# Performance work log

Hardware: AMD Instinct MI355X
Metric: run time of the kernel (lower is better)

Reference implementation:

```python
import jax, jax.numpy as jnp
import numpy as np

N_NODES = 100000
N_EDGES = 1600000
H_DIM = 64  # pos(32) + vel(32)


def _mlp_init(key, d_in, d_hid, d_out):
    k1, k2 = jax.random.split(key)
    s1 = 1.0 / np.sqrt(d_in)
    s2 = 1.0 / np.sqrt(d_hid)
    w1 = jax.random.uniform(k1, (d_in, d_hid), jnp.float32, -s1, s1)
    w2 = jax.random.uniform(k2, (d_hid, d_out), jnp.float32, -s2, s2)
    return w1, jnp.zeros((d_hid,), jnp.float32), w2, jnp.zeros((d_out,), jnp.float32)


def setup_inputs() -> dict:
    key = jax.random.key(0)
    ks = jax.random.split(key, 6)
    pos = jax.random.normal(ks[0], (N_NODES, 32), jnp.float32)
    vel = jax.random.normal(ks[1], (N_NODES, 32), jnp.float32)
    edge_index = jax.random.randint(ks[2], (2, N_EDGES), 0, N_NODES, jnp.int32)
    msg_w1, msg_b1, msg_w2, msg_b2 = _mlp_init(ks[3], 2 * H_DIM, 64, 64)
    upd_w1, upd_b1, upd_w2, upd_b2 = _mlp_init(ks[4], H_DIM + 64, 64, 64)
    sp = 1.0 / np.sqrt(64)
    pred_w = jax.random.uniform(ks[5], (64, 32), jnp.float32, -sp, sp)
    pred_b = jnp.zeros((32,), jnp.float32)
    return dict(pos=pos, vel=vel, edge_index=edge_index,
                msg_w1=msg_w1, msg_b1=msg_b1, msg_w2=msg_w2, msg_b2=msg_b2,
                upd_w1=upd_w1, upd_b1=upd_b1, upd_w2=upd_w2, upd_b2=upd_b2,
                pred_w=pred_w, pred_b=pred_b)


def reference(pos, vel, edge_index,
              msg_w1, msg_b1, msg_w2, msg_b2,
              upd_w1, upd_b1, upd_w2, upd_b2,
              pred_w, pred_b):
    n = pos.shape[0]
    h = jnp.concatenate([pos, vel], axis=-1)              # [N, 64]
    src, dst = edge_index[0], edge_index[1]
    h_i = h[dst]                                          # [E, 64] target nodes
    h_j = h[src]                                          # [E, 64] source nodes
    # message MLP on concat(h_i, h_j)
    m = jnp.concatenate([h_i, h_j], axis=-1)              # [E, 128]
    m = jax.nn.relu(m @ msg_w1 + msg_b1) @ msg_w2 + msg_b2  # [E, 64]
    # scatter-add aggregate to target nodes
    aggr = jax.ops.segment_sum(m, dst, num_segments=n)    # [N, 64]
    # update MLP on concat(h, aggr)
    u = jnp.concatenate([h, aggr], axis=-1)               # [N, 128]
    u = jax.nn.relu(u @ upd_w1 + upd_b1) @ upd_w2 + upd_b2  # [N, 64]
    # linear prediction head -> acceleration
    return u @ pred_w + pred_b                            # [N, 32]
```

## Files before the change

kernel.cpp:

```cpp
#include <hip/hip_runtime.h>

#define NN 100000
#define NE 1600000
#define SB   391
#define NBKT 391
#define EPB  4096

typedef _Float16 f16x8 __attribute__((ext_vector_type(8)));
typedef float    f32x4 __attribute__((ext_vector_type(4)));

#define ZB   1563
#define PHB  3125
#define PWB  13

extern "C" __global__ void __launch_bounds__(256)
prep_kernel(const float* __restrict__ pos, const float* __restrict__ vel,
            const int* __restrict__ ei,
            const float* __restrict__ mw1, const float* __restrict__ mw2,
            const float* __restrict__ uw1, const float* __restrict__ uw2,
            const float* __restrict__ pw,
            _Float16* __restrict__ hh,
            _Float16* __restrict__ mw1f, _Float16* __restrict__ mw2f,
            _Float16* __restrict__ uw1f, _Float16* __restrict__ uw2f,
            _Float16* __restrict__ pwf,
            float* __restrict__ aggr, int* __restrict__ cntm)
{
    __shared__ int lh[NBKT];
    const int b = blockIdx.x, tid = threadIdx.x;
    if (b < ZB) {
        float4* p = (float4*)aggr;
        const int base4 = b * 1024 + tid;
        const float4 z = make_float4(0.f, 0.f, 0.f, 0.f);
#pragma unroll
        for (int k = 0; k < 4; ++k) {
            const int idx = base4 + k * 256;
            if (idx < NN * 16) p[idx] = z;
        }
    } else if (b < ZB + PHB) {
        const int t = (b - ZB) * 256 + tid;
        const int node = t >> 3, seg = t & 7;
        const float* src = (seg < 4) ? pos + (size_t)node * 32 + seg * 8
                                     : vel + (size_t)node * 32 + (seg - 4) * 8;
        const float4 a = ((const float4*)src)[0];
        const float4 c = ((const float4*)src)[1];
        f16x8 r;
        r[0]=(_Float16)a.x; r[1]=(_Float16)a.y; r[2]=(_Float16)a.z; r[3]=(_Float16)a.w;
        r[4]=(_Float16)c.x; r[5]=(_Float16)c.y; r[6]=(_Float16)c.z; r[7]=(_Float16)c.w;
        *(f16x8*)(hh + (size_t)node * 64 + seg * 8) = r;
    } else if (b < ZB + PHB + PWB) {
        const int t2 = (b - ZB - PHB) * 256 + tid;
        if (t2 < 1024) {
            const int t = t2 >> 8, kk = (t2 >> 6) & 3, l = t2 & 63;
            f16x8 r;
#pragma unroll
            for (int j = 0; j < 8; ++j)
                r[j] = (_Float16)mw1[(kk * 32 + (l >> 4) * 8 + j) * 64 + t * 16 + (l & 15)];
            *(f16x8*)(mw1f + (size_t)t2 * 8) = r;
        } else if (t2 < 1536) {
            const int i = t2 - 1024;
            const int t = i >> 7, kk = (i >> 6) & 1, l = i & 63;
            f16x8 r;
#pragma unroll
            for (int j = 0; j < 8; ++j)
                r[j] = (_Float16)mw2[(kk * 32 + (l >> 4) * 8 + j) * 64 + t * 16 + (l & 15)];
            *(f16x8*)(mw2f + (size_t)i * 8) = r;
        } else if (t2 < 2560) {
            const int i = t2 - 1536;
            const int t = i >> 8, kk = (i >> 6) & 3, l = i & 63;
            f16x8 r;
#pragma unroll
            for (int j = 0; j < 8; ++j)
                r[j] = (_Float16)uw1[(kk * 32 + (l >> 4) * 8 + j) * 64 + t * 16 + (l & 15)];
            *(f16x8*)(uw1f + (size_t)i * 8) = r;
        } else if (t2 < 3072) {
            const int i = t2 - 2560;
            const int t = i >> 7, kk = (i >> 6) & 1, l = i & 63;
            f16x8 r;
#pragma unroll
            for (int j = 0; j < 8; ++j)
                r[j] = (_Float16)uw2[(kk * 32 + (l >> 4) * 8 + j) * 64 + t * 16 + (l & 15)];
            *(f16x8*)(uw2f + (size_t)i * 8) = r;
        } else if (t2 < 3328) {
            const int i = t2 - 3072;
            const int t = i >> 7, kk = (i >> 6) & 1, l = i & 63;
            f16x8 r;
#pragma unroll
            for (int j = 0; j < 8; ++j)
                r[j] = (_Float16)pw[(kk * 32 + (l >> 4) * 8 + j) * 32 + t * 16 + (l & 15)];
            *(f16x8*)(pwf + (size_t)i * 8) = r;
        }
    } else {
        const int blk = b - (ZB + PHB + PWB);
        for (int i = tid; i < NBKT; i += 256) lh[i] = 0;
        __syncthreads();
        const int e0 = blk * EPB;
#pragma unroll
        for (int k = 0; k < EPB / 256; ++k) {
            const int e = e0 + k * 256 + tid;
            if (e < NE) atomicAdd(&lh[ei[NE + e] >> 8], 1);
        }
        __syncthreads();
        for (int i = tid; i < NBKT; i += 256) cntm[blk * NBKT + i] = lh[i];
    }
}

extern "C" __global__ void __launch_bounds__(512)
scancol_kernel(const int* __restrict__ cntm, int* __restrict__ gtot,
               int* __restrict__ offs, int* __restrict__ btot,
               int* __restrict__ bbase)
{
    __shared__ int s[512];
    const int tid = threadIdx.x, bkt = blockIdx.x;
    const int v = (tid < SB) ? cntm[tid * NBKT + bkt] : 0;
    s[tid] = v;
    __syncthreads();
    for (int off = 1; off < 512; off <<= 1) {
        int t = (tid >= off) ? s[tid - off] : 0;
        __syncthreads();
        s[tid] += t;
        __syncthreads();
    }
    if (tid < SB) offs[tid * NBKT + bkt] = s[tid] - v;
    if (tid == SB - 1) {
        const int tot = s[tid];
        btot[bkt]  = tot;
        bbase[bkt] = atomicAdd(gtot, tot);
    }
}

extern "C" __global__ void __launch_bounds__(256)
sortC_kernel(const int* __restrict__ ei, const int* __restrict__ offs,
             const int* __restrict__ bbase, int2* __restrict__ sd_tmp)
{
    __shared__ int lh[NBKT];
    __shared__ int lo[NBKT];
    const int tid = threadIdx.x, blk = blockIdx.x;
    for (int i = tid; i < NBKT; i += 256) {
        lh[i] = 0;
        lo[i] = bbase[i] + offs[blk * NBKT + i];
    }
    __syncthreads();
    const int e0 = blk * EPB;
#pragma unroll
    for (int k = 0; k < EPB / 256; ++k) {
        const int e = e0 + k * 256 + tid;
        if (e < NE) {
            const int s = ei[e], d = ei[NE + e];
            const int bkt = d >> 8;
            const int r = atomicAdd(&lh[bkt], 1);
            sd_tmp[lo[bkt] + r] = make_int2(s, d);
        }
    }
}

extern "C" __global__ void __launch_bounds__(256)
sortD_kernel(const int2* __restrict__ sd_tmp, const int* __restrict__ bbase,
             const int* __restrict__ btot, int2* __restrict__ sd2)
{
    __shared__ int h[256];
    __shared__ int s[256];
    __shared__ int dbase[256];
    const int tid = threadIdx.x, bkt = blockIdx.x;
    const int s0 = bbase[bkt];
    const int n  = btot[bkt];
    h[tid] = 0;
    __syncthreads();
    for (int k = tid; k < n; k += 256)
        atomicAdd(&h[sd_tmp[s0 + k].y & 255], 1);
    __syncthreads();
    const int v = h[tid];
    s[tid] = v;
    __syncthreads();
    for (int off = 1; off < 256; off <<= 1) {
        int t = (tid >= off) ? s[tid - off] : 0;
        __syncthreads();
        s[tid] += t;
        __syncthreads();
    }
    dbase[tid] = s[tid] - v;
    __syncthreads();
    h[tid] = 0;
    __syncthreads();
    for (int k = tid; k < n; k += 256) {
        const int2 e = sd_tmp[s0 + k];
        const int dl = e.y & 255;
        const int r = atomicAdd(&h[dl], 1);
        sd2[s0 + dbase[dl] + r] = e;
    }
}

extern "C" __global__ void __launch_bounds__(512, 4)
edgeagg_kernel(const _Float16* __restrict__ hh,
               const int2* __restrict__ sd,
               const _Float16* __restrict__ w1f, const _Float16* __restrict__ w2f,
               const float* __restrict__ b1, const float* __restrict__ b2,
               float* __restrict__ aggr)
{
    __shared__ _Float16 sW1[4 * 4 * 64 * 8];
    __shared__ _Float16 sW2[4 * 2 * 64 * 8];
    __shared__ _Float16 sY[8][16 * 72];

    const int tid = threadIdx.x;
    const int wave = tid >> 6, lane = tid & 63;
    const int m = lane & 15, g = lane >> 4;
    const int wslot = (blockIdx.x * 8 + wave) * 64;

    const int2 sdv = sd[wslot + lane];
    const int prevd = __shfl_up(sdv.y, 1, 64);
    const unsigned long long bmask = __ballot(lane == 0 || sdv.y != prevd);

    {
        const uint4* g1 = (const uint4*)w1f; uint4* s1 = (uint4*)sW1;
        s1[tid] = g1[tid]; s1[512 + tid] = g1[512 + tid];
        const uint4* g2 = (const uint4*)w2f; uint4* s2 = (uint4*)sW2;
        s2[tid] = g2[tid];
    }

    const float bb1[4] = { b1[m], b1[16 + m], b1[32 + m], b1[48 + m] };
    const float bb2[4] = { b2[m], b2[16 + m], b2[32 + m], b2[48 + m] };

    __syncthreads();

    _Float16* Y  = sY[wave];
    _Float16* Yw = Y + g * 4 * 72 + m;
    const _Float16* Yr = Y + m * 72 + g * 8;

    float racc = 0.0f;
    int   rnode = __builtin_amdgcn_readlane(sdv.y, 0);
    int   firstRun = 1;

    f16x8 Abuf[2][4];
    {
        const int ns = __shfl(sdv.x, m, 64);
        const int nd = __shfl(sdv.y, m, 64);
        const _Float16* hd = hh + (size_t)nd * 64 + g * 8;
        const _Float16* hs = hh + (size_t)ns * 64 + g * 8;
        Abuf[0][0] = *(const f16x8*)(hd);
        Abuf[0][1] = *(const f16x8*)(hd + 32);
        Abuf[0][2] = *(const f16x8*)(hs);
        Abuf[0][3] = *(const f16x8*)(hs + 32);
    }

#pragma unroll
    for (int it = 0; it < 4; ++it) {
        const int cur = it & 1;
        if (it < 3) {
            const int ns = __shfl(sdv.x, (it + 1) * 16 + m, 64);
            const int nd = __shfl(sdv.y, (it + 1) * 16 + m, 64);
            const _Float16* hd = hh + (size_t)nd * 64 + g * 8;
            const _Float16* hs = hh + (size_t)ns * 64 + g * 8;
            Abuf[cur ^ 1][0] = *(const f16x8*)(hd);
            Abuf[cur ^ 1][1] = *(const f16x8*)(hd + 32);
            Abuf[cur ^ 1][2] = *(const f16x8*)(hs);
            Abuf[cur ^ 1][3] = *(const f16x8*)(hs + 32);
        }

        f32x4 acc[4];
#pragma unroll
        for (int t = 0; t < 4; ++t) {
            acc[t][0] = bb1[t]; acc[t][1] = bb1[t];
            acc[t][2] = bb1[t]; acc[t][3] = bb1[t];
        }
#pragma unroll
        for (int t = 0; t < 4; ++t) {
#pragma unroll
            for (int kk = 0; kk < 4; ++kk) {
                const f16x8 b = *(const f16x8*)(sW1 + ((t * 4 + kk) * 64 + lane) * 8);
                acc[t] = __builtin_amdgcn_mfma_f32_16x16x32_f16(Abuf[cur][kk], b, acc[t], 0, 0, 0);
            }
        }

        __builtin_amdgcn_sched_barrier(0);
#pragma unroll
        for (int t = 0; t < 4; ++t) {
#pragma unroll
            for (int r = 0; r < 4; ++r)
                Yw[r * 72 + t * 16] = (_Float16)fmaxf(acc[t][r], 0.0f);
        }
        __builtin_amdgcn_sched_barrier(0);

        f16x8 a2[2];
        a2[0] = *(const f16x8*)(Yr);
        a2[1] = *(const f16x8*)(Yr + 32);

        f32x4 acc2[4];
#pragma unroll
        for (int t = 0; t < 4; ++t) {
            acc2[t][0] = bb2[t]; acc2[t][1] = bb2[t];
            acc2[t][2] = bb2[t]; acc2[t][3] = bb2[t];
        }
#pragma unroll
        for (int kk = 0; kk < 2; ++kk) {
#pragma unroll
            for (int t = 0; t < 4; ++t) {
                const f16x8 b = *(const f16x8*)(sW2 + ((t * 2 + kk) * 64 + lane) * 8);
                acc2[t] = __builtin_amdgcn_mfma_f32_16x16x32_f16(a2[kk], b, acc2[t], 0, 0, 0);
            }
        }

        const unsigned tm = (unsigned)((bmask >> (it * 16)) & 0xFFFFull) | 0x10000u;
        if (tm == 0x10000u) {
            float p0 = 0.f, p1 = 0.f, p2 = 0.f, p3 = 0.f;
#pragma unroll
            for (int r = 0; r < 4; ++r) {
                p0 += acc2[0][r]; p1 += acc2[1][r];
                p2 += acc2[2][r]; p3 += acc2[3][r];
            }
            p0 += __shfl_xor(p0, 16); p0 += __shfl_xor(p0, 32);
            p1 += __shfl_xor(p1, 16); p1 += __shfl_xor(p1, 32);
            p2 += __shfl_xor(p2, 16); p2 += __shfl_xor(p2, 32);
            p3 += __shfl_xor(p3, 16); p3 += __shfl_xor(p3, 32);
            racc += (g == 0) ? p0 : (g == 1) ? p1 : (g == 2) ? p2 : p3;
        } else {
            int a = 0;
            while (a < 16) {
                const int b = a + 1 + __builtin_ctz(tm >> (a + 1));
                const int d = __builtin_amdgcn_readlane(sdv.y, it * 16 + a);
                if (d != rnode) {
                    float* ap = aggr + (size_t)rnode * 64 + lane;
                    if (firstRun) atomicAdd(ap, racc);
                    else          *ap = racc;
                    firstRun = 0; racc = 0.0f; rnode = d;
                }
                float p0 = 0.f, p1 = 0.f, p2 = 0.f, p3 = 0.f;
#pragma unroll
                for (int r = 0; r < 4; ++r) {
                    const int rowl = 4 * g + r;
                    const bool in = (rowl >= a) && (rowl < b);
                    p0 += in ? acc2[0][r] : 0.f;
                    p1 += in ? acc2[1][r] : 0.f;
                    p2 += in ? acc2[2][r] : 0.f;
                    p3 += in ? acc2[3][r] : 0.f;
                }
                p0 += __shfl_xor(p0, 16); p0 += __shfl_xor(p0, 32);
                p1 += __shfl_xor(p1, 16); p1 += __shfl_xor(p1, 32);
                p2 += __shfl_xor(p2, 16); p2 += __shfl_xor(p2, 32);
                p3 += __shfl_xor(p3, 16); p3 += __shfl_xor(p3, 32);
                racc += (g == 0) ? p0 : (g == 1) ? p1 : (g == 2) ? p2 : p3;
                a = b;
            }
        }
    }
    atomicAdd(aggr + (size_t)rnode * 64 + lane, racc);
}

extern "C" __global__ void __launch_bounds__(256)
node_mfma_kernel(const _Float16* __restrict__ hh, const float* __restrict__ aggr,
                 const _Float16* __restrict__ uw1f, const _Float16* __restrict__ uw2f,
                 const _Float16* __restrict__ pwf,
                 const float* __restrict__ b1, const float* __restrict__ b2,
                 const float* __restrict__ pb, float* __restrict__ out)
{
    __shared__ _Float16 sU1[4 * 4 * 64 * 8];
    __shared__ _Float16 sU2[4 * 2 * 64 * 8];
    __shared__ _Float16 sPW[2 * 2 * 64 * 8];
    __shared__ _Float16 sT[4][16 * 64];

    const int tid = threadIdx.x;
    {
        const uint4* g1 = (const uint4*)uw1f; uint4* s1 = (uint4*)sU1;
#pragma unroll
        for (int i = 0; i < 4; ++i) s1[i * 256 + tid] = g1[i * 256 + tid];
        const uint4* g2 = (const uint4*)uw2f; uint4* s2 = (uint4*)sU2;
#pragma unroll
        for (int i = 0; i < 2; ++i) s2[i * 256 + tid] = g2[i * 256 + tid];
        const uint4* g3 = (const uint4*)pwf;  uint4* s3 = (uint4*)sPW;
        s3[tid] = g3[tid];
    }
    __syncthreads();

    const int wave = tid >> 6, lane = tid & 63;
    const int m = lane & 15, g = lane >> 4;
    const int nb = (blockIdx.x * 4 + wave) * 16;
    const int v = nb + m;
    const int vl = (v < NN) ? v : (NN - 1);

    const _Float16* hv = hh + (size_t)vl * 64 + g * 8;
    const f16x8 a0 = *(const f16x8*)(hv);
    const f16x8 a1 = *(const f16x8*)(hv + 32);
    const float* av = aggr + (size_t)vl * 64 + g * 8;
    const float4 x0 = *(const float4*)(av),      x1 = *(const float4*)(av + 4);
    const float4 y0 = *(const float4*)(av + 32), y1 = *(const float4*)(av + 36);
    f16x8 a2, a3;
    a2[0]=(_Float16)x0.x; a2[1]=(_Float16)x0.y; a2[2]=(_Float16)x0.z; a2[3]=(_Float16)x0.w;
    a2[4]=(_Float16)x1.x; a2[5]=(_Float16)x1.y; a2[6]=(_Float16)x1.z; a2[7]=(_Float16)x1.w;
    a3[0]=(_Float16)y0.x; a3[1]=(_Float16)y0.y; a3[2]=(_Float16)y0.z; a3[3]=(_Float16)y0.w;
    a3[4]=(_Float16)y1.x; a3[5]=(_Float16)y1.y; a3[6]=(_Float16)y1.z; a3[7]=(_Float16)y1.w;

    f32x4 acc[4] = {};
#pragma unroll
    for (int t = 0; t < 4; ++t) {
        acc[t] = __builtin_amdgcn_mfma_f32_16x16x32_f16(
            a0, *(const f16x8*)(sU1 + ((t * 4 + 0) * 64 + lane) * 8), acc[t], 0, 0, 0);
        acc[t] = __builtin_amdgcn_mfma_f32_16x16x32_f16(
            a1, *(const f16x8*)(sU1 + ((t * 4 + 1) * 64 + lane) * 8), acc[t], 0, 0, 0);
        acc[t] = __builtin_amdgcn_mfma_f32_16x16x32_f16(
            a2, *(const f16x8*)(sU1 + ((t * 4 + 2) * 64 + lane) * 8), acc[t], 0, 0, 0);
        acc[t] = __builtin_amdgcn_mfma_f32_16x16x32_f16(
            a3, *(const f16x8*)(sU1 + ((t * 4 + 3) * 64 + lane) * 8), acc[t], 0, 0, 0);
    }

    _Float16* Y = sT[wave];
#pragma unroll
    for (int t = 0; t < 4; ++t) {
        const float bb = b1[t * 16 + m];
#pragma unroll
        for (int r = 0; r < 4; ++r) {
            const float y = fmaxf(acc[t][r] + bb, 0.0f);
            const int row = g * 4 + r, col = t * 16 + m;
            const int byteoff = row * 128 + ((2 * col) ^ ((row & 7) << 4));
            *(_Float16*)((char*)Y + byteoff) = (_Float16)y;
        }
    }
    asm volatile("s_waitcnt lgkmcnt(0)" ::: "memory");
    __builtin_amdgcn_sched_barrier(0);

    f16x8 ay[2];
#pragma unroll
    for (int kk = 0; kk < 2; ++kk) {
        const int c = kk * 4 + g;
        ay[kk] = *(const f16x8*)((char*)Y + m * 128 + ((c * 16) ^ ((m & 7) << 4)));
    }
    asm volatile("s_waitcnt lgkmcnt(0)" ::: "memory");
    __builtin_amdgcn_sched_barrier(0);

    f32x4 acc2[4] = {};
#pragma unroll
    for (int kk = 0; kk < 2; ++kk) {
#pragma unroll
        for (int t = 0; t < 4; ++t) {
            const f16x8 b = *(const f16x8*)(sU2 + ((t * 2 + kk) * 64 + lane) * 8);
            acc2[t] = __builtin_amdgcn_mfma_f32_16x16x32_f16(ay[kk], b, acc2[t], 0, 0, 0);
        }
    }

#pragma unroll
    for (int t = 0; t < 4; ++t) {
        const float bb = b2[t * 16 + m];
#pragma unroll
        for (int r = 0; r < 4; ++r) {
            const float u = acc2[t][r] + bb;
            const int row = g * 4 + r, col = t * 16 + m;
            const int byteoff = row * 128 + ((2 * col) ^ ((row & 7) << 4));
            *(_Float16*)((char*)Y + byteoff) = (_Float16)u;
        }
    }
    asm volatile("s_waitcnt lgkmcnt(0)" ::: "memory");
    __builtin_amdgcn_sched_barrier(0);

    f16x8 au[2];
#pragma unroll
    for (int kk = 0; kk < 2; ++kk) {
        const int c = kk * 4 + g;
        au[kk] = *(const f16x8*)((char*)Y + m * 128 + ((c * 16) ^ ((m & 7) << 4)));
    }
    asm volatile("s_waitcnt lgkmcnt(0)" ::: "memory");
    __builtin_amdgcn_sched_barrier(0);

    f32x4 acc3[2] = {};
#pragma unroll
    for (int kk = 0; kk < 2; ++kk) {
#pragma unroll
        for (int t = 0; t < 2; ++t) {
            const f16x8 b = *(const f16x8*)(sPW + ((t * 2 + kk) * 64 + lane) * 8);
            acc3[t] = __builtin_amdgcn_mfma_f32_16x16x32_f16(au[kk], b, acc3[t], 0, 0, 0);
        }
    }

    float* F = (float*)Y;
#pragma unroll
    for (int t = 0; t < 2; ++t) {
        const float bb = pb[t * 16 + m];
#pragma unroll
        for (int r = 0; r < 4; ++r) {
            const int row = g * 4 + r, col = t * 16 + m;
            const int byteoff = row * 128 + ((4 * col) ^ ((row & 7) << 4));
            *(float*)((char*)F + byteoff) = acc3[t][r] + bb;
        }
    }
    asm volatile("s_waitcnt lgkmcnt(0)" ::: "memory");
    __builtin_amdgcn_sched_barrier(0);

    const int row = lane >> 2, q = lane & 3;
    const float4 o0 = *(const float4*)((char*)F + row * 128 + ((q * 16)       ^ ((row & 7) << 4)));
    const float4 o1 = *(const float4*)((char*)F + row * 128 + (((q + 4) * 16) ^ ((row & 7) << 4)));
    if (nb + row < NN) {
        float4* op = (float4*)(out + (size_t)(nb + row) * 32);
        op[q]     = o0;
        op[q + 4] = o1;
    }
}

extern "C" __global__ void __launch_bounds__(256)
edge_msg_kernel(const float* __restrict__ pos, const float* __restrict__ vel,
                const int* __restrict__ ei,
                const float* __restrict__ w1, const float* __restrict__ b1,
                const float* __restrict__ w2, const float* __restrict__ b2,
                float* __restrict__ aggr)
{
    const int e = blockIdx.x * 256 + threadIdx.x;
    if (e >= NE) return;
    const int ns = ei[e];
    const int nd = ei[NE + e];
    float y[64];
#pragma unroll
    for (int j = 0; j < 64; ++j) y[j] = b1[j];
    for (int part = 0; part < 4; ++part) {
        const int    node  = (part < 2) ? nd : ns;
        const float* basep = (part & 1) ? vel : pos;
        const float4* xp = reinterpret_cast<const float4*>(basep + (size_t)node * 32);
        const float*  wp = w1 + part * 32 * 64;
        for (int q = 0; q < 8; ++q) {
            const float4 xv = xp[q];
#pragma unroll
            for (int kk = 0; kk < 4; ++kk) {
                const float xs = (kk == 0) ? xv.x : (kk == 1) ? xv.y
                               : (kk == 2) ? xv.z : xv.w;
                const float* wr = wp + (q * 4 + kk) * 64;
#pragma unroll
                for (int j = 0; j < 64; ++j) y[j] = fmaf(xs, wr[j], y[j]);
            }
        }
    }
    float mm[64];
#pragma unroll
    for (int c = 0; c < 64; ++c) mm[c] = b2[c];
#pragma unroll
    for (int j = 0; j < 64; ++j) {
        const float yj = fmaxf(y[j], 0.0f);
        const float* wr = w2 + j * 64;
#pragma unroll
        for (int c = 0; c < 64; ++c) mm[c] = fmaf(yj, wr[c], mm[c]);
    }
    float* ap = aggr + (size_t)nd * 64;
#pragma unroll
    for (int c = 0; c < 64; ++c) atomicAdd(ap + c, mm[c]);
}

extern "C" __global__ void __launch_bounds__(256)
node_upd_kernel(const float* __restrict__ pos, const float* __restrict__ vel,
                const float* __restrict__ aggr,
                const float* __restrict__ w1, const float* __restrict__ b1,
                const float* __restrict__ w2, const float* __restrict__ b2,
                const float* __restrict__ pw, const float* __restrict__ pb,
                float* __restrict__ out)
{
    const int v = blockIdx.x * 256 + threadIdx.x;
    if (v >= NN) return;

    float y[64];
#pragma unroll
    for (int j = 0; j < 64; ++j) y[j] = b1[j];
    for (int part = 0; part < 4; ++part) {
        const float* basep = (part == 0) ? pos + (size_t)v * 32
                           : (part == 1) ? vel + (size_t)v * 32
                           : aggr + (size_t)v * 64 + (size_t)(part - 2) * 32;
        const float4* xp = reinterpret_cast<const float4*>(basep);
        const float*  wp = w1 + part * 32 * 64;
        for (int q = 0; q < 8; ++q) {
            const float4 xv = xp[q];
#pragma unroll
            for (int kk = 0; kk < 4; ++kk) {
                const float xs = (kk == 0) ? xv.x : (kk == 1) ? xv.y
                               : (kk == 2) ? xv.z : xv.w;
                const float* wr = wp + (q * 4 + kk) * 64;
#pragma unroll
                for (int j = 0; j < 64; ++j) y[j] = fmaf(xs, wr[j], y[j]);
            }
        }
    }

    float u[64];
#pragma unroll
    for (int c = 0; c < 64; ++c) u[c] = b2[c];
#pragma unroll
    for (int j = 0; j < 64; ++j) {
        const float yj = fmaxf(y[j], 0.0f);
        const float* wr = w2 + j * 64;
#pragma unroll
        for (int c = 0; c < 64; ++c) u[c] = fmaf(yj, wr[c], u[c]);
    }

    float o[32];
#pragma unroll
    for (int c = 0; c < 32; ++c) o[c] = pb[c];
#pragma unroll
    for (int j = 0; j < 64; ++j) {
        const float* wr = pw + j * 32;
#pragma unroll
        for (int c = 0; c < 32; ++c) o[c] = fmaf(u[j], wr[c], o[c]);
    }

    float4* op = reinterpret_cast<float4*>(out + (size_t)v * 32);
#pragma unroll
    for (int q = 0; q < 8; ++q)
        op[q] = make_float4(o[q * 4], o[q * 4 + 1], o[q * 4 + 2], o[q * 4 + 3]);
}

extern "C" void kernel_launch(void* const* d_in, const int* in_sizes, int n_in,
                              void* d_out, int out_size, void* d_ws, size_t ws_size,
                              hipStream_t stream)
{
    const float* pos = (const float*)d_in[0];
    const float* vel = (const float*)d_in[1];
    const int*   ei  = (const int*)d_in[2];
    const float* mw1 = (const float*)d_in[3];
    const float* mb1 = (const float*)d_in[4];
    const float* mw2 = (const float*)d_in[5];
    const float* mb2 = (const float*)d_in[6];
    const float* uw1 = (const float*)d_in[7];
    const float* ub1 = (const float*)d_in[8];
    const float* uw2 = (const float*)d_in[9];
    const float* ub2 = (const float*)d_in[10];
    const float* pw  = (const float*)d_in[11];
    const float* pb  = (const float*)d_in[12];
    float* out = (float*)d_out;

    char* ws = (char*)d_ws;
    size_t off = 0;
    float*    aggr   = (float*)(ws + off);    off += (size_t)NN * 64 * 4;
    _Float16* hh     = (_Float16*)(ws + off); off += (size_t)NN * 64 * 2;
    int2*     sd_tmp = (int2*)(ws + off);     off += (size_t)NE * 8;
    int2*     sd2    = (int2*)(ws + off);     off += (size_t)NE * 8;
    int*      cntm   = (int*)(ws + off);      off += (size_t)SB * NBKT * 4;
    int*      offs   = (int*)(ws + off);      off += (size_t)SB * NBKT * 4;
    int*      btot   = (int*)(ws + off);      off += 512 * 4;
    int*      bbase  = (int*)(ws + off);      off += 512 * 4;
    int*      gtot   = (int*)(ws + off);      off += 256;
    _Float16* mw1f   = (_Float16*)(ws + off); off += 1024 * 8 * 2;
    _Float16* mw2f   = (_Float16*)(ws + off); off += 512 * 8 * 2;
    _Float16* uw1f   = (_Float16*)(ws + off); off += 1024 * 8 * 2;
    _Float16* uw2f   = (_Float16*)(ws + off); off += 512 * 8 * 2;
    _Float16* pwf    = (_Float16*)(ws + off); off += 256 * 8 * 2;
    const size_t need_full = off;

    if (ws_size >= need_full) {
        hipMemsetAsync(gtot, 0, sizeof(int), stream);
        prep_kernel<<<ZB + PHB + PWB + SB, 256, 0, stream>>>(
            pos, vel, ei, mw1, mw2, uw1, uw2, pw,
            hh, mw1f, mw2f, uw1f, uw2f, pwf, aggr, cntm);
        scancol_kernel<<<NBKT, 512, 0, stream>>>(cntm, gtot, offs, btot, bbase);
        sortC_kernel<<<SB, 256, 0, stream>>>(ei, offs, bbase, sd_tmp);
        sortD_kernel<<<NBKT, 256, 0, stream>>>(sd_tmp, bbase, btot, sd2);
        edgeagg_kernel<<<NE / 512, 512, 0, stream>>>(
            hh, sd2, mw1f, mw2f, mb1, mb2, aggr);
        node_mfma_kernel<<<(NN + 63) / 64, 256, 0, stream>>>(
            hh, aggr, uw1f, uw2f, pwf, ub1, ub2, pb, out);
    } else {
        float* aggr2 = (float*)d_ws;
        hipMemsetAsync(aggr2, 0, (size_t)NN * 64 * sizeof(float), stream);
        edge_msg_kernel<<<NE / 256, 256, 0, stream>>>(pos, vel, ei,
                                                      mw1, mb1, mw2, mb2, aggr2);
        node_upd_kernel<<<(NN + 255) / 256, 256, 0, stream>>>(
            pos, vel, aggr2, uw1, ub1, uw2, ub2, pw, pb, out);
    }
}
```

Before: 143.8 us.

## Triple-buffer edge gathers, XOR-swizzle hidden-layer LDS tile, raise MFMA priority

Deepens the gather prefetch in the edge-MLP kernel from double to triple buffering, so node feature loads are issued two tiles ahead of the MFMA work. The padded 72-stride LDS staging tile for the ReLU hidden layer becomes an unpadded 64-wide tile with an XOR swizzle to avoid bank conflicts, and explicit lgkmcnt waits are added. s_setprio is raised around MFMA blocks to favour matrix issue across waves. Using more registers for the extra buffer may lower occupancy under the 512x4 launch bound.

```diff
diff --git a/kernel.cpp b/kernel.cpp
--- a/kernel.cpp
+++ b/kernel.cpp
@@ -198,7 +198,7 @@
 {
     __shared__ _Float16 sW1[4 * 4 * 64 * 8];
     __shared__ _Float16 sW2[4 * 2 * 64 * 8];
-    __shared__ _Float16 sY[8][16 * 72];
+    __shared__ _Float16 sT[8][16 * 64];
 
     const int tid = threadIdx.x;
     const int wave = tid >> 6, lane = tid & 63;
@@ -221,38 +221,38 @@
 
     __syncthreads();
 
-    _Float16* Y  = sY[wave];
-    _Float16* Yw = Y + g * 4 * 72 + m;
-    const _Float16* Yr = Y + m * 72 + g * 8;
+    _Float16* Y = sT[wave];
 
     float racc = 0.0f;
     int   rnode = __builtin_amdgcn_readlane(sdv.y, 0);
     int   firstRun = 1;
 
-    f16x8 Abuf[2][4];
-    {
-        const int ns = __shfl(sdv.x, m, 64);
-        const int nd = __shfl(sdv.y, m, 64);
+    f16x8 Abuf[3][4];
+#pragma unroll
+    for (int p = 0; p < 2; ++p) {
+        const int ns = __shfl(sdv.x, p * 16 + m, 64);
+        const int nd = __shfl(sdv.y, p * 16 + m, 64);
         const _Float16* hd = hh + (size_t)nd * 64 + g * 8;
         const _Float16* hs = hh + (size_t)ns * 64 + g * 8;
-        Abuf[0][0] = *(const f16x8*)(hd);
-        Abuf[0][1] = *(const f16x8*)(hd + 32);
-        Abuf[0][2] = *(const f16x8*)(hs);
-        Abuf[0][3] = *(const f16x8*)(hs + 32);
+        Abuf[p][0] = *(const f16x8*)(hd);
+        Abuf[p][1] = *(const f16x8*)(hd + 32);
+        Abuf[p][2] = *(const f16x8*)(hs);
+        Abuf[p][3] = *(const f16x8*)(hs + 32);
     }
 
 #pragma unroll
     for (int it = 0; it < 4; ++it) {
-        const int cur = it & 1;
-        if (it < 3) {
-            const int ns = __shfl(sdv.x, (it + 1) * 16 + m, 64);
-            const int nd = __shfl(sdv.y, (it + 1) * 16 + m, 64);
+        const int cur = it % 3;
+        if (it < 2) {
+            const int nxt = (it + 2) % 3;
+            const int ns = __shfl(sdv.x, (it + 2) * 16 + m, 64);
+            const int nd = __shfl(sdv.y, (it + 2) * 16 + m, 64);
             const _Float16* hd = hh + (size_t)nd * 64 + g * 8;
             const _Float16* hs = hh + (size_t)ns * 64 + g * 8;
-            Abuf[cur ^ 1][0] = *(const f16x8*)(hd);
-            Abuf[cur ^ 1][1] = *(const f16x8*)(hd + 32);
-            Abuf[cur ^ 1][2] = *(const f16x8*)(hs);
-            Abuf[cur ^ 1][3] = *(const f16x8*)(hs + 32);
+            Abuf[nxt][0] = *(const f16x8*)(hd);
+            Abuf[nxt][1] = *(const f16x8*)(hd + 32);
+            Abuf[nxt][2] = *(const f16x8*)(hs);
+            Abuf[nxt][3] = *(const f16x8*)(hs + 32);
         }
 
         f32x4 acc[4];
@@ -261,6 +261,7 @@
             acc[t][0] = bb1[t]; acc[t][1] = bb1[t];
             acc[t][2] = bb1[t]; acc[t][3] = bb1[t];
         }
+        __builtin_amdgcn_s_setprio(1);
 #pragma unroll
         for (int t = 0; t < 4; ++t) {
 #pragma unroll
@@ -269,19 +270,29 @@
                 acc[t] = __builtin_amdgcn_mfma_f32_16x16x32_f16(Abuf[cur][kk], b, acc[t], 0, 0, 0);
             }
         }
-
+        __builtin_amdgcn_s_setprio(0);
+
+#pragma unroll
+        for (int t = 0; t < 4; ++t) {
+#pragma unroll
+            for (int r = 0; r < 4; ++r) {
+                const float y = fmaxf(acc[t][r], 0.0f);
+                const int row = g * 4 + r, col = t * 16 + m;
+                const int byteoff = row * 128 + ((2 * col) ^ ((row & 7) << 4));
+                *(_Float16*)((char*)Y + byteoff) = (_Float16)y;
+            }
+        }
+        asm volatile("s_waitcnt lgkmcnt(0)" ::: "memory");
         __builtin_amdgcn_sched_barrier(0);
-#pragma unroll
-        for (int t = 0; t < 4; ++t) {
-#pragma unroll
-            for (int r = 0; r < 4; ++r)
-                Yw[r * 72 + t * 16] = (_Float16)fmaxf(acc[t][r], 0.0f);
-        }
+
+        f16x8 a2[2];
+#pragma unroll
+        for (int kk = 0; kk < 2; ++kk) {
+            const int c = kk * 4 + g;
+            a2[kk] = *(const f16x8*)((char*)Y + m * 128 + ((c * 16) ^ ((m & 7) << 4)));
+        }
+        asm volatile("s_waitcnt lgkmcnt(0)" ::: "memory");
         __builtin_amdgcn_sched_barrier(0);
-
-        f16x8 a2[2];
-        a2[0] = *(const f16x8*)(Yr);
-        a2[1] = *(const f16x8*)(Yr + 32);
 
         f32x4 acc2[4];
 #pragma unroll
@@ -289,6 +300,7 @@
             acc2[t][0] = bb2[t]; acc2[t][1] = bb2[t];
             acc2[t][2] = bb2[t]; acc2[t][3] = bb2[t];
         }
+        __builtin_amdgcn_s_setprio(1);
 #pragma unroll
         for (int kk = 0; kk < 2; ++kk) {
 #pragma unroll
@@ -297,6 +309,7 @@
                 acc2[t] = __builtin_amdgcn_mfma_f32_16x16x32_f16(a2[kk], b, acc2[t], 0, 0, 0);
             }
         }
+        __builtin_amdgcn_s_setprio(0);
 
         const unsigned tm = (unsigned)((bmask >> (it * 16)) & 0xFFFFull) | 0x10000u;
         if (tm == 0x10000u) {
```

Result: slower. 161.6 us (+12.4%).
